# Performance work log

Measured on AMD Instinct MI355X. Metric: run time of the kernel, lower is better.

## Reference

```python
import jax, jax.numpy as jnp
import numpy as np

B, H, S, DH = 1, 16, 4096, 128
D_MODEL = H * DH  # 2048


def setup_inputs() -> dict:
    key = jax.random.key(0)
    kq, kk, kv = jax.random.split(key, 3)
    q = jax.random.normal(kq, (B, H, S, DH), dtype=jnp.float32)
    k = jax.random.normal(kk, (B, H, S, DH), dtype=jnp.float32)
    v = jax.random.normal(kv, (B, H, S, DH), dtype=jnp.float32)
    # causal mask: 1 where attending is allowed, 0 elsewhere (masked_fill on ==0)
    attn_mask = jnp.tril(jnp.ones((S, S), dtype=jnp.int32))[None, None, :, :]
    return {"q": q, "k": k, "v": v, "seq_length": S, "attn_mask": attn_mask}


def reference(q, k, v, seq_length, attn_mask):
    # q,k,v: [1, H, S, DH]; attn_mask: [1, 1, S, S] (0 = masked)
    scale = 1.0 / jnp.sqrt(jnp.asarray(q.shape[-1], dtype=q.dtype))
    att = jnp.einsum("bhqd,bhkd->bhqk", q, k) * scale  # [1,H,S,S]
    mask = attn_mask[:, :, :seq_length, :seq_length]
    att = jnp.where(mask == 0, jnp.asarray(-jnp.inf, dtype=att.dtype), att)
    att = jax.nn.softmax(att, axis=-1)
    y = jnp.einsum("bhqk,bhkd->bhqd", att, v)  # [1,H,S,DH]
    # transpose(1,2) -> [1,S,H,DH] -> view(S, d_model)
    y = jnp.transpose(y, (0, 2, 1, 3)).reshape(seq_length, H * DH)
    return y
```

## Files before the change

### kernel.cpp

```cpp
#include <hip/hip_runtime.h>

#define HH 16
#define SS 4096
#define DHD 128
#define BR 64
#define BC 64
#define LDQS 136
#define LDQ 144
#define LDV 68
#define LDPT 72
#define LDOS 136
#define DM  (HH * DHD)

typedef __bf16 bf16x8_t __attribute__((ext_vector_type(8)));
typedef __bf16 bf16x4_t __attribute__((ext_vector_type(4)));
typedef float  f32x4_t  __attribute__((ext_vector_type(4)));

#define BAR()  asm volatile("s_waitcnt lgkmcnt(0)\n\ts_barrier" ::: "memory")
#define BARV() asm volatile("s_waitcnt vmcnt(0)\n\ts_barrier" ::: "memory")

typedef __attribute__((address_space(1))) const void gas_t;
typedef __attribute__((address_space(3))) void las_t;
__device__ __forceinline__ void gl16(const void* g, void* l) {
    __builtin_amdgcn_global_load_lds((gas_t*)g, (las_t*)l, 16, 0, 0);
}

__device__ __forceinline__ f32x4_t vmax4(f32x4_t a, f32x4_t b) {
    f32x4_t r;
    r[0] = fmaxf(a[0], b[0]); r[1] = fmaxf(a[1], b[1]);
    r[2] = fmaxf(a[2], b[2]); r[3] = fmaxf(a[3], b[3]);
    return r;
}

__global__ __launch_bounds__(256)
void prep_k(const float* __restrict__ k, __bf16* __restrict__ wk)
{
    const int c0 = (blockIdx.x * 256 + threadIdx.x) * 4;
    #pragma unroll
    for (int i = 0; i < 4; ++i) {
        const int c    = c0 + i;
        const int tile = c >> 10;
        const int o    = (c & 1023) * 16;
        const int row  = o >> 8;
        const int e0   = (o & 255) >> 1;
        const int scol = e0 ^ ((row & 7) << 3);
        const float* src = k + (((size_t)(tile * 64 + row)) << 7) + scol;
        float4 a = ((const float4*)src)[0];
        float4 b = ((const float4*)src)[1];
        bf16x8_t bb;
        bb[0] = (__bf16)a.x; bb[1] = (__bf16)a.y; bb[2] = (__bf16)a.z; bb[3] = (__bf16)a.w;
        bb[4] = (__bf16)b.x; bb[5] = (__bf16)b.y; bb[6] = (__bf16)b.z; bb[7] = (__bf16)b.w;
        *(bf16x8_t*)((char*)wk + (size_t)c * 16) = bb;
    }
}

__global__ __launch_bounds__(256)
void prep_v(const float* __restrict__ v, __bf16* __restrict__ wv)
{
    __shared__ __bf16 lt[64 * 132];
    const int tile = blockIdx.x;
    const int tid  = threadIdx.x;
    #pragma unroll
    for (int i = 0; i < 8; ++i) {
        int idx = tid + i * 256;
        int r = idx >> 5, cc = idx & 31;
        float4 val = ((const float4*)(v + (((size_t)(tile * 64 + r)) << 7)))[cc];
        bf16x4_t bb;
        bb[0] = (__bf16)val.x; bb[1] = (__bf16)val.y;
        bb[2] = (__bf16)val.z; bb[3] = (__bf16)val.w;
        *(bf16x4_t*)&lt[r * 132 + cc * 4] = bb;
    }
    __syncthreads();
    #pragma unroll
    for (int i = 0; i < 4; ++i) {
        int ch = tid * 4 + i;
        int o  = ch * 8;
        int d  = o >> 6;
        int e0 = o & 63;
        int ks = e0 ^ ((d & 7) << 3);
        bf16x8_t bb;
        #pragma unroll
        for (int z = 0; z < 8; ++z) bb[z] = lt[(ks + z) * 132 + d];
        *(bf16x8_t*)((char*)wv + (size_t)tile * 16384 + (size_t)o * 2) = bb;
    }
}

__global__ __launch_bounds__(256, 2)
void fa_fwd(const float* __restrict__ q, const __bf16* __restrict__ wk,
            const __bf16* __restrict__ wv, float* __restrict__ out)
{
    const int L = blockIdx.x;
    const int h = L & 15;
    const int g = L >> 4;
    const int qts[2] = { g, 63 - g };

    const int tid  = threadIdx.x;
    const int wave = tid >> 6;
    const int lane = tid & 63;
    const int l16  = lane & 15;
    const int quad = lane >> 4;
    const int rK   = tid >> 5;
    const int c4   = tid & 31;
    const int swz  = (l16 & 7) << 4;

    __shared__ __align__(16) char smem[74752];
    unsigned short* pT_s = (unsigned short*)(smem + 65536);
    unsigned short* q_s  = (unsigned short*)(smem + 32768);
    float* os = (float*)smem;

    const float* qh = q + (size_t)h * SS * DHD;

    auto stage = [&](int j, int b) {
        const size_t tb = ((size_t)(h * 64 + j)) * 16384;
        const char* gk = (const char*)wk + tb + wave * 4096 + lane * 16;
        const char* gv = (const char*)wv + tb + wave * 4096 + lane * 16;
        char* lk = smem + b * 16384 + wave * 4096;
        char* lv = smem + 32768 + b * 16384 + wave * 4096;
        #pragma unroll
        for (int c2 = 0; c2 < 4; ++c2) {
            gl16(gk + c2 * 1024, lk + c2 * 1024);
            gl16(gv + c2 * 1024, lv + c2 * 1024);
        }
    };

    const float scale = 0.088388347648318447f * 1.4426950408889634f;

    for (int t = 0; t < 2; ++t) {
        const int qt = qts[t];
        __syncthreads();
        #pragma unroll
        for (int i = 0; i < 8; ++i) {
            int idx = tid + i * 256;
            int r   = idx >> 5;
            int cc  = idx & 31;
            float4 val = ((const float4*)(qh + (size_t)(qt * BR + r) * DHD))[cc];
            bf16x4_t bb;
            bb[0] = (__bf16)(val.x * scale); bb[1] = (__bf16)(val.y * scale);
            bb[2] = (__bf16)(val.z * scale); bb[3] = (__bf16)(val.w * scale);
            *(bf16x4_t*)&q_s[r * LDQS + cc * 4] = bb;
        }
        __syncthreads();

        bf16x8_t qf[4];
        #pragma unroll
        for (int kc = 0; kc < 4; ++kc)
            qf[kc] = *(const bf16x8_t*)
                &q_s[(wave * 16 + l16) * LDQS + kc * 32 + quad * 8];
        BAR();

        stage(0, 0);

        f32x4_t oacc[8];
        #pragma unroll
        for (int mt = 0; mt < 8; ++mt) oacc[mt] = (f32x4_t)(0.0f);
        float mi = -INFINITY, li = 0.0f;

        const int q_local = wave * 16 + l16;

        for (int j = 0; j <= qt; ++j) {
            const int cur = j & 1;
            BARV();
            if (j < qt) stage(j + 1, cur ^ 1);

            const char* kb = smem + cur * 16384;
            const char* vb = smem + 32768 + cur * 16384;

            f32x4_t sa[4];
            #pragma unroll
            for (int mt = 0; mt < 4; ++mt) sa[mt] = (f32x4_t)(0.0f);
            __builtin_amdgcn_s_setprio(1);
            #pragma unroll
            for (int kc = 0; kc < 4; ++kc)
                #pragma unroll
                for (int mt = 0; mt < 4; ++mt) {
                    bf16x8_t kf = *(const bf16x8_t*)
                        (kb + (mt * 16 + l16) * 256 + ((kc * 64 + quad * 16) ^ swz));
                    sa[mt] = __builtin_amdgcn_mfma_f32_16x16x32_bf16(kf, qf[kc], sa[mt], 0, 0, 0);
                }
            __builtin_amdgcn_s_setprio(0);

            if (j == qt) {
                #pragma unroll
                for (int mt = 0; mt < 4; ++mt)
                    #pragma unroll
                    for (int r = 0; r < 4; ++r)
                        if (mt * 16 + quad * 4 + r > q_local) sa[mt][r] = -INFINITY;
            }

            f32x4_t mv = vmax4(vmax4(sa[0], sa[1]), vmax4(sa[2], sa[3]));
            float mx = fmaxf(fmaxf(mv[0], mv[1]), fmaxf(mv[2], mv[3]));
            mx = fmaxf(mx, __shfl_xor(mx, 16));
            mx = fmaxf(mx, __shfl_xor(mx, 32));
            const bool skip = __all((int)(mx <= mi + 8.0f)) != 0;
            const float mnew = skip ? mi : fmaxf(mi, mx);
            bf16x4_t pkv[4];
            #pragma unroll
            for (int mt = 0; mt < 4; ++mt) {
                #pragma unroll
                for (int r = 0; r < 4; ++r)
                    sa[mt][r] = __builtin_amdgcn_exp2f(sa[mt][r] - mnew);
                pkv[mt][0] = (__bf16)sa[mt][0]; pkv[mt][1] = (__bf16)sa[mt][1];
                pkv[mt][2] = (__bf16)sa[mt][2]; pkv[mt][3] = (__bf16)sa[mt][3];
            }
            f32x4_t sv = sa[0] + sa[1] + sa[2] + sa[3];
            float rs = (sv[0] + sv[1]) + (sv[2] + sv[3]);
            rs += __shfl_xor(rs, 16);
            rs += __shfl_xor(rs, 32);
            if (skip) {
                li += rs;
            } else {
                float a = __builtin_amdgcn_exp2f(mi - mnew);
                mi = mnew;
                li = li * a + rs;
                #pragma unroll
                for (int mt = 0; mt < 8; ++mt) {
                    oacc[mt][0] *= a; oacc[mt][1] *= a;
                    oacc[mt][2] *= a; oacc[mt][3] *= a;
                }
            }

            #pragma unroll
            for (int mt = 0; mt < 4; ++mt)
                *(bf16x4_t*)&pT_s[q_local * LDPT + mt * 16 + quad * 4] = pkv[mt];

            __builtin_amdgcn_s_setprio(1);
            #pragma unroll
            for (int kc = 0; kc < 2; ++kc) {
                bf16x8_t pb = *(const bf16x8_t*)
                    &pT_s[q_local * LDPT + kc * 32 + quad * 8];
                #pragma unroll
                for (int mt = 0; mt < 8; ++mt) {
                    bf16x8_t vf = *(const bf16x8_t*)
                        (vb + (mt * 16 + l16) * 128 + ((kc * 64 + quad * 16) ^ swz));
                    oacc[mt] = __builtin_amdgcn_mfma_f32_16x16x32_bf16(vf, pb, oacc[mt], 0, 0, 0);
                }
            }
            __builtin_amdgcn_s_setprio(0);
        }

        __syncthreads();
        float inv = 1.0f / li;
        #pragma unroll
        for (int mt = 0; mt < 8; ++mt)
            #pragma unroll
            for (int r = 0; r < 4; ++r)
                os[(wave * 16 + l16) * LDOS + mt * 16 + quad * 4 + r] = oacc[mt][r] * inv;
        __syncthreads();
        #pragma unroll
        for (int p = 0; p < 8; ++p) {
            int row = p * 8 + rK;
            float4 f4 = *(const float4*)&os[row * LDOS + c4 * 4];
            *(float4*)&out[(size_t)(qts[t] * BR + row) * DM + h * DHD + c4 * 4] = f4;
        }
    }
}

__global__ __launch_bounds__(256, 2)
void fa_fwd_fb(const float* __restrict__ q, const float* __restrict__ k,
               const float* __restrict__ v, float* __restrict__ out)
{
    const int L = blockIdx.x;
    const int h = L & 15;
    const int g = L >> 4;
    const int qts[2] = { g, 63 - g };

    const int tid  = threadIdx.x;
    const int wave = tid >> 6;
    const int lane = tid & 63;
    const int l16  = lane & 15;
    const int quad = lane >> 4;
    const int rK   = tid >> 5;
    const int c4   = tid & 31;
    const int dbase = (wave & 1) * 64;
    const int rbase = (wave >> 1) * 32;

    __shared__ __align__(16) char smem[63488];
    unsigned short* qp_s = (unsigned short*)smem;
    unsigned short* k_s  = (unsigned short*)(smem + 18432);
    unsigned short* vt_s = (unsigned short*)(smem + 36864);
    unsigned short* pT_s = (unsigned short*)(smem + 54272);
    float* os = (float*)smem;

    const size_t hoff = (size_t)h * SS * DHD;
    const float* qh = q + hoff;
    const float* kh = k + hoff;
    const float* vh = v + hoff;

    float4 kreg[8];
    float  vreg[8][4];
    auto issue = [&](int j) {
        const float* kb = kh + (size_t)j * BC * DHD;
        #pragma unroll
        for (int i = 0; i < 8; ++i)
            kreg[i] = ((const float4*)(kb + (size_t)(rK + i * 8) * DHD))[c4];
        const float* vb = vh + (size_t)j * BC * DHD + dbase + lane;
        #pragma unroll
        for (int p = 0; p < 8; ++p) {
            const float* vp = vb + (size_t)(rbase + p * 4) * DHD;
            vreg[p][0] = vp[0];
            vreg[p][1] = vp[DHD];
            vreg[p][2] = vp[2 * DHD];
            vreg[p][3] = vp[3 * DHD];
        }
    };

    const float scale = 0.088388347648318447f;
    issue(0);

    for (int t = 0; t < 2; ++t) {
        const int qt = qts[t];
        __syncthreads();
        #pragma unroll
        for (int i = 0; i < 8; ++i) {
            int idx = tid + i * 256;
            int r   = idx >> 5;
            int cc  = idx & 31;
            float4 val = ((const float4*)(qh + (size_t)(qt * BR + r) * DHD))[cc];
            bf16x4_t bb;
            bb[0] = (__bf16)(val.x * scale); bb[1] = (__bf16)(val.y * scale);
            bb[2] = (__bf16)(val.z * scale); bb[3] = (__bf16)(val.w * scale);
            *(bf16x4_t*)&qp_s[r * LDQ + cc * 4] = bb;
        }
        __syncthreads();

        bf16x8_t qf[4];
        #pragma unroll
        for (int kc = 0; kc < 4; ++kc)
            qf[kc] = *(const bf16x8_t*)
                &qp_s[(wave * 16 + l16) * LDQ + kc * 32 + quad * 8];

        f32x4_t oacc[8];
        #pragma unroll
        for (int mt = 0; mt < 8; ++mt) oacc[mt] = (f32x4_t)(0.0f);
        float mi = -INFINITY, li = 0.0f;
        const int q_local = wave * 16 + l16;

        for (int j = 0; j <= qt; ++j) {
            BAR();
            #pragma unroll
            for (int i = 0; i < 8; ++i) {
                bf16x4_t bb;
                bb[0] = (__bf16)kreg[i].x; bb[1] = (__bf16)kreg[i].y;
                bb[2] = (__bf16)kreg[i].z; bb[3] = (__bf16)kreg[i].w;
                *(bf16x4_t*)&k_s[(rK + i * 8) * LDQ + c4 * 4] = bb;
            }
            #pragma unroll
            for (int p = 0; p < 8; ++p) {
                bf16x4_t bb;
                bb[0] = (__bf16)vreg[p][0]; bb[1] = (__bf16)vreg[p][1];
                bb[2] = (__bf16)vreg[p][2]; bb[3] = (__bf16)vreg[p][3];
                *(bf16x4_t*)&vt_s[(dbase + lane) * LDV + rbase + p * 4] = bb;
            }
            if (j < qt)      issue(j + 1);
            else if (t == 0) issue(0);
            BAR();

            f32x4_t sa[4];
            #pragma unroll
            for (int mt = 0; mt < 4; ++mt) sa[mt] = (f32x4_t)(0.0f);
            #pragma unroll
            for (int kc = 0; kc < 4; ++kc)
                #pragma unroll
                for (int mt = 0; mt < 4; ++mt) {
                    bf16x8_t kf = *(const bf16x8_t*)
                        &k_s[(mt * 16 + l16) * LDQ + kc * 32 + quad * 8];
                    sa[mt] = __builtin_amdgcn_mfma_f32_16x16x32_bf16(kf, qf[kc], sa[mt], 0, 0, 0);
                }

            if (j == qt) {
                #pragma unroll
                for (int mt = 0; mt < 4; ++mt)
                    #pragma unroll
                    for (int r = 0; r < 4; ++r)
                        if (mt * 16 + quad * 4 + r > q_local) sa[mt][r] = -INFINITY;
            }

            f32x4_t mv = vmax4(vmax4(sa[0], sa[1]), vmax4(sa[2], sa[3]));
            float mx = fmaxf(fmaxf(mv[0], mv[1]), fmaxf(mv[2], mv[3]));
            mx = fmaxf(mx, __shfl_xor(mx, 16));
            mx = fmaxf(mx, __shfl_xor(mx, 32));
            float mnew = fmaxf(mi, mx);
            float a = __expf(mi - mnew);
            mi = mnew;
            bf16x4_t pkv[4];
            #pragma unroll
            for (int mt = 0; mt < 4; ++mt) {
                #pragma unroll
                for (int r = 0; r < 4; ++r) sa[mt][r] = __expf(sa[mt][r] - mnew);
                pkv[mt][0] = (__bf16)sa[mt][0]; pkv[mt][1] = (__bf16)sa[mt][1];
                pkv[mt][2] = (__bf16)sa[mt][2]; pkv[mt][3] = (__bf16)sa[mt][3];
            }
            f32x4_t sv = sa[0] + sa[1] + sa[2] + sa[3];
            float rs = (sv[0] + sv[1]) + (sv[2] + sv[3]);
            rs += __shfl_xor(rs, 16);
            rs += __shfl_xor(rs, 32);
            li = li * a + rs;

            #pragma unroll
            for (int mt = 0; mt < 4; ++mt)
                *(bf16x4_t*)&pT_s[(wave * 16 + l16) * LDPT + mt * 16 + quad * 4] = pkv[mt];

            #pragma unroll
            for (int mt = 0; mt < 8; ++mt) {
                oacc[mt][0] *= a; oacc[mt][1] *= a;
                oacc[mt][2] *= a; oacc[mt][3] *= a;
            }

            #pragma unroll
            for (int kc = 0; kc < 2; ++kc) {
                bf16x8_t pb = *(const bf16x8_t*)
                    &pT_s[(wave * 16 + l16) * LDPT + kc * 32 + quad * 8];
                #pragma unroll
                for (int mt = 0; mt < 8; ++mt) {
                    bf16x4_t vlo = *(const bf16x4_t*)
                        &vt_s[(mt * 16 + l16) * LDV + kc * 32 + quad * 8];
                    bf16x4_t vhi = *(const bf16x4_t*)
                        &vt_s[(mt * 16 + l16) * LDV + kc * 32 + quad * 8 + 4];
                    bf16x8_t vf = __builtin_shufflevector(vlo, vhi, 0,1,2,3,4,5,6,7);
                    oacc[mt] = __builtin_amdgcn_mfma_f32_16x16x32_bf16(vf, pb, oacc[mt], 0, 0, 0);
                }
            }
        }

        __syncthreads();
        float inv = 1.0f / li;
        #pragma unroll
        for (int mt = 0; mt < 8; ++mt)
            #pragma unroll
            for (int r = 0; r < 4; ++r)
                os[(wave * 16 + l16) * LDOS + mt * 16 + quad * 4 + r] = oacc[mt][r] * inv;
        __syncthreads();
        #pragma unroll
        for (int p = 0; p < 8; ++p) {
            int row = p * 8 + rK;
            float4 f4 = *(const float4*)&os[row * LDOS + c4 * 4];
            *(float4*)&out[(size_t)(qt * BR + row) * DM + h * DHD + c4 * 4] = f4;
        }
    }
}

extern "C" void kernel_launch(void* const* d_in, const int* in_sizes, int n_in,
                              void* d_out, int out_size, void* d_ws, size_t ws_size,
                              hipStream_t stream) {
    const float* q = (const float*)d_in[0];
    const float* k = (const float*)d_in[1];
    const float* v = (const float*)d_in[2];
    float* out = (float*)d_out;
    if (d_ws != nullptr && ws_size >= (size_t)33554432) {
        __bf16* wk = (__bf16*)d_ws;
        __bf16* wv = (__bf16*)((char*)d_ws + 16777216);
        prep_k<<<dim3(1024), dim3(256), 0, stream>>>(k, wk);
        prep_v<<<dim3(1024), dim3(256), 0, stream>>>(v, wv);
        fa_fwd<<<dim3((SS / BR / 2) * HH), dim3(256), 0, stream>>>(q, wk, wv, out);
    } else {
        fa_fwd_fb<<<dim3((SS / BR / 2) * HH), dim3(256), 0, stream>>>(q, k, v, out);
    }
}
```

Before: 289.6 us.

## Software-pipeline QK^T one tile ahead with split K/V staging

Splits K and V loads into separate stages so that K is prefetched two tiles ahead and V one tile ahead. The loop is restructured to compute the next tile's QK^T scores while the current tile's softmax and PV run, ping-ponging between two score register sets. The row-sum reduction is deferred to the end, and the max shuffle now runs only when the rescale is not skipped. This hides LDS and MFMA latency behind softmax work, at the cost of more registers, which may hurt occupancy under the two-blocks-per-SIMD launch bound.

```diff
diff --git a/kernel.cpp b/kernel.cpp
--- a/kernel.cpp
+++ b/kernel.cpp
@@ -11,6 +11,7 @@
 #define LDPT 72
 #define LDOS 136
 #define DM  (HH * DHD)
+#define KTILE 16384
 
 typedef __bf16 bf16x8_t __attribute__((ext_vector_type(8)));
 typedef __bf16 bf16x4_t __attribute__((ext_vector_type(4)));
@@ -110,24 +111,98 @@
 
     const float* qh = q + (size_t)h * SS * DHD;
 
-    auto stage = [&](int j, int b) {
-        const size_t tb = ((size_t)(h * 64 + j)) * 16384;
-        const char* gk = (const char*)wk + tb + wave * 4096 + lane * 16;
-        const char* gv = (const char*)wv + tb + wave * 4096 + lane * 16;
-        char* lk = smem + b * 16384 + wave * 4096;
-        char* lv = smem + 32768 + b * 16384 + wave * 4096;
-        #pragma unroll
-        for (int c2 = 0; c2 < 4; ++c2) {
-            gl16(gk + c2 * 1024, lk + c2 * 1024);
-            gl16(gv + c2 * 1024, lv + c2 * 1024);
-        }
+    auto stageK = [&](int j, int b) {
+        const char* gk = (const char*)wk + ((size_t)(h * 64 + j)) * KTILE + wave * 4096 + lane * 16;
+        char* lk = smem + b * KTILE + wave * 4096;
+        #pragma unroll
+        for (int c2 = 0; c2 < 4; ++c2) gl16(gk + c2 * 1024, lk + c2 * 1024);
     };
+    auto stageV = [&](int j, int b) {
+        const char* gv = (const char*)wv + ((size_t)(h * 64 + j)) * KTILE + wave * 4096 + lane * 16;
+        char* lv = smem + 32768 + b * KTILE + wave * 4096;
+        #pragma unroll
+        for (int c2 = 0; c2 < 4; ++c2) gl16(gv + c2 * 1024, lv + c2 * 1024);
+    };
 
     const float scale = 0.088388347648318447f * 1.4426950408889634f;
+
+#define ITER(SC, SN) do {                                                     \
+    if (j + 2 <= qt) stageK(j + 2, j & 1);                                    \
+    if (j + 1 <= qt) stageV(j + 1, (j + 1) & 1);                              \
+    if (j < qt) {                                                             \
+        const char* kbp = smem + ((j + 1) & 1) * KTILE;                       \
+        _Pragma("unroll")                                                     \
+        for (int mt = 0; mt < 4; ++mt) SN[mt] = (f32x4_t)(0.0f);              \
+        __builtin_amdgcn_s_setprio(1);                                        \
+        _Pragma("unroll")                                                     \
+        for (int kc = 0; kc < 4; ++kc)                                        \
+            _Pragma("unroll")                                                 \
+            for (int mt = 0; mt < 4; ++mt) {                                  \
+                bf16x8_t kf = *(const bf16x8_t*)                              \
+                    (kbp + (mt * 16 + l16) * 256 + ((kc * 64 + quad * 16) ^ swz)); \
+                SN[mt] = __builtin_amdgcn_mfma_f32_16x16x32_bf16(kf, qf[kc], SN[mt], 0, 0, 0); \
+            }                                                                 \
+        __builtin_amdgcn_s_setprio(0);                                        \
+    }                                                                         \
+    if (j == qt) {                                                            \
+        _Pragma("unroll")                                                     \
+        for (int mt = 0; mt < 4; ++mt)                                        \
+            _Pragma("unroll")                                                 \
+            for (int r = 0; r < 4; ++r)                                       \
+                if (mt * 16 + quad * 4 + r > q_local) SC[mt][r] = -INFINITY;  \
+    }                                                                         \
+    f32x4_t mv = vmax4(vmax4(SC[0], SC[1]), vmax4(SC[2], SC[3]));             \
+    float mxl = fmaxf(fmaxf(mv[0], mv[1]), fmaxf(mv[2], mv[3]));              \
+    const bool skip = __all((int)(mxl <= mi + 8.0f)) != 0;                    \
+    float mnew = mi;                                                          \
+    if (!skip) {                                                              \
+        float mr = fmaxf(mxl, __shfl_xor(mxl, 16));                           \
+        mr = fmaxf(mr, __shfl_xor(mr, 32));                                   \
+        mnew = fmaxf(mi, mr);                                                 \
+        float a = __builtin_amdgcn_exp2f(mi - mnew);                          \
+        mi = mnew;                                                            \
+        li *= a;                                                              \
+        _Pragma("unroll")                                                     \
+        for (int mt = 0; mt < 8; ++mt) {                                      \
+            oacc[mt][0] *= a; oacc[mt][1] *= a;                               \
+            oacc[mt][2] *= a; oacc[mt][3] *= a;                               \
+        }                                                                     \
+    }                                                                         \
+    bf16x4_t pkv[4];                                                          \
+    _Pragma("unroll")                                                         \
+    for (int mt = 0; mt < 4; ++mt) {                                          \
+        _Pragma("unroll")                                                     \
+        for (int r = 0; r < 4; ++r)                                           \
+            SC[mt][r] = __builtin_amdgcn_exp2f(SC[mt][r] - mnew);             \
+        pkv[mt][0] = (__bf16)SC[mt][0]; pkv[mt][1] = (__bf16)SC[mt][1];       \
+        pkv[mt][2] = (__bf16)SC[mt][2]; pkv[mt][3] = (__bf16)SC[mt][3];       \
+        *(bf16x4_t*)&pT_s[q_local * LDPT + mt * 16 + quad * 4] = pkv[mt];     \
+    }                                                                         \
+    f32x4_t sv = SC[0] + SC[1] + SC[2] + SC[3];                               \
+    li += (sv[0] + sv[1]) + (sv[2] + sv[3]);                                  \
+    {                                                                         \
+        const char* vbp = smem + 32768 + (j & 1) * KTILE;                     \
+        __builtin_amdgcn_s_setprio(1);                                        \
+        _Pragma("unroll")                                                     \
+        for (int kc = 0; kc < 2; ++kc) {                                      \
+            bf16x8_t pb = *(const bf16x8_t*)&pT_s[q_local * LDPT + kc * 32 + quad * 8]; \
+            _Pragma("unroll")                                                 \
+            for (int mt = 0; mt < 8; ++mt) {                                  \
+                bf16x8_t vf = *(const bf16x8_t*)                              \
+                    (vbp + (mt * 16 + l16) * 128 + ((kc * 64 + quad * 16) ^ swz)); \
+                oacc[mt] = __builtin_amdgcn_mfma_f32_16x16x32_bf16(vf, pb, oacc[mt], 0, 0, 0); \
+            }                                                                 \
+        }                                                                     \
+        __builtin_amdgcn_s_setprio(0);                                        \
+    }                                                                         \
+    BARV();                                                                   \
+} while (0)
 
     for (int t = 0; t < 2; ++t) {
         const int qt = qts[t];
         __syncthreads();
+        stageK(0, 0);
+        stageK(1, 1);
         #pragma unroll
         for (int i = 0; i < 8; ++i) {
             int idx = tid + i * 256;
@@ -147,96 +222,43 @@
             qf[kc] = *(const bf16x8_t*)
                 &q_s[(wave * 16 + l16) * LDQS + kc * 32 + quad * 8];
         BAR();
-
-        stage(0, 0);
+        stageV(0, 0);
 
         f32x4_t oacc[8];
         #pragma unroll
         for (int mt = 0; mt < 8; ++mt) oacc[mt] = (f32x4_t)(0.0f);
         float mi = -INFINITY, li = 0.0f;
-
         const int q_local = wave * 16 + l16;
 
-        for (int j = 0; j <= qt; ++j) {
-            const int cur = j & 1;
-            BARV();
-            if (j < qt) stage(j + 1, cur ^ 1);
-
-            const char* kb = smem + cur * 16384;
-            const char* vb = smem + 32768 + cur * 16384;
-
-            f32x4_t sa[4];
-            #pragma unroll
-            for (int mt = 0; mt < 4; ++mt) sa[mt] = (f32x4_t)(0.0f);
+        BARV();
+
+        f32x4_t sA[4], sB[4];
+        {
+            const char* kbp = smem;
+            #pragma unroll
+            for (int mt = 0; mt < 4; ++mt) sA[mt] = (f32x4_t)(0.0f);
             __builtin_amdgcn_s_setprio(1);
             #pragma unroll
             for (int kc = 0; kc < 4; ++kc)
                 #pragma unroll
                 for (int mt = 0; mt < 4; ++mt) {
                     bf16x8_t kf = *(const bf16x8_t*)
-                        (kb + (mt * 16 + l16) * 256 + ((kc * 64 + quad * 16) ^ swz));
-                    sa[mt] = __builtin_amdgcn_mfma_f32_16x16x32_bf16(kf, qf[kc], sa[mt], 0, 0, 0);
+                        (kbp + (mt * 16 + l16) * 256 + ((kc * 64 + quad * 16) ^ swz));
+                    sA[mt] = __builtin_amdgcn_mfma_f32_16x16x32_bf16(kf, qf[kc], sA[mt], 0, 0, 0);
                 }
             __builtin_amdgcn_s_setprio(0);
-
-            if (j == qt) {
-                #pragma unroll
-                for (int mt = 0; mt < 4; ++mt)
-                    #pragma unroll
-                    for (int r = 0; r < 4; ++r)
-                        if (mt * 16 + quad * 4 + r > q_local) sa[mt][r] = -INFINITY;
-            }
-
-            f32x4_t mv = vmax4(vmax4(sa[0], sa[1]), vmax4(sa[2], sa[3]));
-            float mx = fmaxf(fmaxf(mv[0], mv[1]), fmaxf(mv[2], mv[3]));
-            mx = fmaxf(mx, __shfl_xor(mx, 16));
-            mx = fmaxf(mx, __shfl_xor(mx, 32));
-            const bool skip = __all((int)(mx <= mi + 8.0f)) != 0;
-            const float mnew = skip ? mi : fmaxf(mi, mx);
-            bf16x4_t pkv[4];
-            #pragma unroll
-            for (int mt = 0; mt < 4; ++mt) {
-                #pragma unroll
-                for (int r = 0; r < 4; ++r)
-                    sa[mt][r] = __builtin_amdgcn_exp2f(sa[mt][r] - mnew);
-                pkv[mt][0] = (__bf16)sa[mt][0]; pkv[mt][1] = (__bf16)sa[mt][1];
-                pkv[mt][2] = (__bf16)sa[mt][2]; pkv[mt][3] = (__bf16)sa[mt][3];
-            }
-            f32x4_t sv = sa[0] + sa[1] + sa[2] + sa[3];
-            float rs = (sv[0] + sv[1]) + (sv[2] + sv[3]);
-            rs += __shfl_xor(rs, 16);
-            rs += __shfl_xor(rs, 32);
-            if (skip) {
-                li += rs;
-            } else {
-                float a = __builtin_amdgcn_exp2f(mi - mnew);
-                mi = mnew;
-                li = li * a + rs;
-                #pragma unroll
-                for (int mt = 0; mt < 8; ++mt) {
-                    oacc[mt][0] *= a; oacc[mt][1] *= a;
-                    oacc[mt][2] *= a; oacc[mt][3] *= a;
-                }
-            }
-
-            #pragma unroll
-            for (int mt = 0; mt < 4; ++mt)
-                *(bf16x4_t*)&pT_s[q_local * LDPT + mt * 16 + quad * 4] = pkv[mt];
-
-            __builtin_amdgcn_s_setprio(1);
-            #pragma unroll
-            for (int kc = 0; kc < 2; ++kc) {
-                bf16x8_t pb = *(const bf16x8_t*)
-                    &pT_s[q_local * LDPT + kc * 32 + quad * 8];
-                #pragma unroll
-                for (int mt = 0; mt < 8; ++mt) {
-                    bf16x8_t vf = *(const bf16x8_t*)
-                        (vb + (mt * 16 + l16) * 128 + ((kc * 64 + quad * 16) ^ swz));
-                    oacc[mt] = __builtin_amdgcn_mfma_f32_16x16x32_bf16(vf, pb, oacc[mt], 0, 0, 0);
-                }
-            }
-            __builtin_amdgcn_s_setprio(0);
-        }
+        }
+
+        int j = 0;
+        for (;;) {
+            ITER(sA, sB);
+            if (j == qt) break; ++j;
+            ITER(sB, sA);
+            if (j == qt) break; ++j;
+        }
+
+        li += __shfl_xor(li, 16);
+        li += __shfl_xor(li, 32);
 
         __syncthreads();
         float inv = 1.0f / li;
@@ -250,9 +272,10 @@
         for (int p = 0; p < 8; ++p) {
             int row = p * 8 + rK;
             float4 f4 = *(const float4*)&os[row * LDOS + c4 * 4];
-            *(float4*)&out[(size_t)(qts[t] * BR + row) * DM + h * DHD + c4 * 4] = f4;
-        }
-    }
+            *(float4*)&out[(size_t)(qt * BR + row) * DM + h * DHD + c4 * 4] = f4;
+        }
+    }
+#undef ITER
 }
 
 __global__ __launch_bounds__(256, 2)
```

New measurement: 271.3 us. 6.3% less time.

## Load K/V MFMA fragments directly from global into registers, drop LDS staging

Applied to the files above, without the earlier changes.

Prep kernels now write K and V in MFMA fragment order so each wave loads its 16 K and 16 V bf16x8 fragments straight from global memory into registers. The LDS double buffer, global_load_lds staging and per-tile barriers go away, and the next tile is prefetched after each MFMA phase. Row-sum shuffles are deferred to the end of the loop and the max shuffle runs only when rescaling. Launch bounds drop to one block per SIMD set because of the higher register use. Each wave now loads the full K/V tile itself, so global/L2 traffic rises fourfold, and occupancy falls.

```diff
diff --git a/kernel.cpp b/kernel.cpp
--- a/kernel.cpp
+++ b/kernel.cpp
@@ -17,13 +17,6 @@
 typedef float  f32x4_t  __attribute__((ext_vector_type(4)));
 
 #define BAR()  asm volatile("s_waitcnt lgkmcnt(0)\n\ts_barrier" ::: "memory")
-#define BARV() asm volatile("s_waitcnt vmcnt(0)\n\ts_barrier" ::: "memory")
-
-typedef __attribute__((address_space(1))) const void gas_t;
-typedef __attribute__((address_space(3))) void las_t;
-__device__ __forceinline__ void gl16(const void* g, void* l) {
-    __builtin_amdgcn_global_load_lds((gas_t*)g, (las_t*)l, 16, 0, 0);
-}
 
 __device__ __forceinline__ f32x4_t vmax4(f32x4_t a, f32x4_t b) {
     f32x4_t r;
@@ -40,11 +33,12 @@
     for (int i = 0; i < 4; ++i) {
         const int c    = c0 + i;
         const int tile = c >> 10;
-        const int o    = (c & 1023) * 16;
-        const int row  = o >> 8;
-        const int e0   = (o & 255) >> 1;
-        const int scol = e0 ^ ((row & 7) << 3);
-        const float* src = k + (((size_t)(tile * 64 + row)) << 7) + scol;
+        const int idx  = c & 1023;
+        const int f    = idx >> 6;
+        const int ln   = idx & 63;
+        const int row  = (f & 3) * 16 + (ln & 15);
+        const int col  = (f >> 2) * 32 + (ln >> 4) * 8;
+        const float* src = k + (((size_t)(tile * 64 + row)) << 7) + col;
         float4 a = ((const float4*)src)[0];
         float4 b = ((const float4*)src)[1];
         bf16x8_t bb;
@@ -73,19 +67,19 @@
     __syncthreads();
     #pragma unroll
     for (int i = 0; i < 4; ++i) {
-        int ch = tid * 4 + i;
-        int o  = ch * 8;
-        int d  = o >> 6;
-        int e0 = o & 63;
-        int ks = e0 ^ ((d & 7) << 3);
+        int idx = tid * 4 + i;
+        int f   = idx >> 6;
+        int ln  = idx & 63;
+        int d   = (f & 7) * 16 + (ln & 15);
+        int kidx = (f >> 3) * 32 + (ln >> 4) * 8;
         bf16x8_t bb;
         #pragma unroll
-        for (int z = 0; z < 8; ++z) bb[z] = lt[(ks + z) * 132 + d];
-        *(bf16x8_t*)((char*)wv + (size_t)tile * 16384 + (size_t)o * 2) = bb;
-    }
-}
-
-__global__ __launch_bounds__(256, 2)
+        for (int z = 0; z < 8; ++z) bb[z] = lt[(kidx + z) * 132 + d];
+        *(bf16x8_t*)((char*)wv + (size_t)tile * 16384 + (size_t)idx * 16) = bb;
+    }
+}
+
+__global__ __launch_bounds__(256, 1)
 void fa_fwd(const float* __restrict__ q, const __bf16* __restrict__ wk,
             const __bf16* __restrict__ wv, float* __restrict__ out)
 {
@@ -101,26 +95,27 @@
     const int quad = lane >> 4;
     const int rK   = tid >> 5;
     const int c4   = tid & 31;
-    const int swz  = (l16 & 7) << 4;
-
-    __shared__ __align__(16) char smem[74752];
-    unsigned short* pT_s = (unsigned short*)(smem + 65536);
-    unsigned short* q_s  = (unsigned short*)(smem + 32768);
+
+    __shared__ __align__(16) char smem[44032];
+    unsigned short* q_s  = (unsigned short*)smem;
+    unsigned short* pT_s = (unsigned short*)(smem + 34816);
     float* os = (float*)smem;
 
     const float* qh = q + (size_t)h * SS * DHD;
-
-    auto stage = [&](int j, int b) {
-        const size_t tb = ((size_t)(h * 64 + j)) * 16384;
-        const char* gk = (const char*)wk + tb + wave * 4096 + lane * 16;
-        const char* gv = (const char*)wv + tb + wave * 4096 + lane * 16;
-        char* lk = smem + b * 16384 + wave * 4096;
-        char* lv = smem + 32768 + b * 16384 + wave * 4096;
-        #pragma unroll
-        for (int c2 = 0; c2 < 4; ++c2) {
-            gl16(gk + c2 * 1024, lk + c2 * 1024);
-            gl16(gv + c2 * 1024, lv + c2 * 1024);
-        }
+    const bf16x8_t* kh8 = (const bf16x8_t*)wk + (size_t)h * 64 * 1024 + lane;
+    const bf16x8_t* vh8 = (const bf16x8_t*)wv + (size_t)h * 64 * 1024 + lane;
+
+    bf16x8_t kf[16];
+    bf16x8_t vf[16];
+    auto ldk = [&](int j) {
+        const bf16x8_t* p = kh8 + (size_t)j * 1024;
+        #pragma unroll
+        for (int f = 0; f < 16; ++f) kf[f] = p[f * 64];
+    };
+    auto ldv = [&](int j) {
+        const bf16x8_t* p = vh8 + (size_t)j * 1024;
+        #pragma unroll
+        for (int f = 0; f < 16; ++f) vf[f] = p[f * 64];
     };
 
     const float scale = 0.088388347648318447f * 1.4426950408889634f;
@@ -128,6 +123,9 @@
     for (int t = 0; t < 2; ++t) {
         const int qt = qts[t];
         __syncthreads();
+        ldk(0);
+        ldv(0);
+
         #pragma unroll
         for (int i = 0; i < 8; ++i) {
             int idx = tid + i * 256;
@@ -146,25 +144,14 @@
         for (int kc = 0; kc < 4; ++kc)
             qf[kc] = *(const bf16x8_t*)
                 &q_s[(wave * 16 + l16) * LDQS + kc * 32 + quad * 8];
-        BAR();
-
-        stage(0, 0);
 
         f32x4_t oacc[8];
         #pragma unroll
         for (int mt = 0; mt < 8; ++mt) oacc[mt] = (f32x4_t)(0.0f);
         float mi = -INFINITY, li = 0.0f;
-
         const int q_local = wave * 16 + l16;
 
         for (int j = 0; j <= qt; ++j) {
-            const int cur = j & 1;
-            BARV();
-            if (j < qt) stage(j + 1, cur ^ 1);
-
-            const char* kb = smem + cur * 16384;
-            const char* vb = smem + 32768 + cur * 16384;
-
             f32x4_t sa[4];
             #pragma unroll
             for (int mt = 0; mt < 4; ++mt) sa[mt] = (f32x4_t)(0.0f);
@@ -172,12 +159,11 @@
             #pragma unroll
             for (int kc = 0; kc < 4; ++kc)
                 #pragma unroll
-                for (int mt = 0; mt < 4; ++mt) {
-                    bf16x8_t kf = *(const bf16x8_t*)
-                        (kb + (mt * 16 + l16) * 256 + ((kc * 64 + quad * 16) ^ swz));
-                    sa[mt] = __builtin_amdgcn_mfma_f32_16x16x32_bf16(kf, qf[kc], sa[mt], 0, 0, 0);
-                }
+                for (int mt = 0; mt < 4; ++mt)
+                    sa[mt] = __builtin_amdgcn_mfma_f32_16x16x32_bf16(
+                        kf[kc * 4 + mt], qf[kc], sa[mt], 0, 0, 0);
             __builtin_amdgcn_s_setprio(0);
+            if (j < qt) ldk(j + 1);
 
             if (j == qt) {
                 #pragma unroll
@@ -188,11 +174,22 @@
             }
 
             f32x4_t mv = vmax4(vmax4(sa[0], sa[1]), vmax4(sa[2], sa[3]));
-            float mx = fmaxf(fmaxf(mv[0], mv[1]), fmaxf(mv[2], mv[3]));
-            mx = fmaxf(mx, __shfl_xor(mx, 16));
-            mx = fmaxf(mx, __shfl_xor(mx, 32));
-            const bool skip = __all((int)(mx <= mi + 8.0f)) != 0;
-            const float mnew = skip ? mi : fmaxf(mi, mx);
+            float mxl = fmaxf(fmaxf(mv[0], mv[1]), fmaxf(mv[2], mv[3]));
+            const bool skip = __all((int)(mxl <= mi + 8.0f)) != 0;
+            float mnew = mi;
+            if (!skip) {
+                float mr = fmaxf(mxl, __shfl_xor(mxl, 16));
+                mr = fmaxf(mr, __shfl_xor(mr, 32));
+                mnew = fmaxf(mi, mr);
+                float a = __builtin_amdgcn_exp2f(mi - mnew);
+                mi = mnew;
+                li *= a;
+                #pragma unroll
+                for (int mt = 0; mt < 8; ++mt) {
+                    oacc[mt][0] *= a; oacc[mt][1] *= a;
+                    oacc[mt][2] *= a; oacc[mt][3] *= a;
+                }
+            }
             bf16x4_t pkv[4];
             #pragma unroll
             for (int mt = 0; mt < 4; ++mt) {
@@ -201,27 +198,10 @@
                     sa[mt][r] = __builtin_amdgcn_exp2f(sa[mt][r] - mnew);
                 pkv[mt][0] = (__bf16)sa[mt][0]; pkv[mt][1] = (__bf16)sa[mt][1];
                 pkv[mt][2] = (__bf16)sa[mt][2]; pkv[mt][3] = (__bf16)sa[mt][3];
+                *(bf16x4_t*)&pT_s[q_local * LDPT + mt * 16 + quad * 4] = pkv[mt];
             }
             f32x4_t sv = sa[0] + sa[1] + sa[2] + sa[3];
-            float rs = (sv[0] + sv[1]) + (sv[2] + sv[3]);
-            rs += __shfl_xor(rs, 16);
-            rs += __shfl_xor(rs, 32);
-            if (skip) {
-                li += rs;
-            } else {
-                float a = __builtin_amdgcn_exp2f(mi - mnew);
-                mi = mnew;
-                li = li * a + rs;
-                #pragma unroll
-                for (int mt = 0; mt < 8; ++mt) {
-                    oacc[mt][0] *= a; oacc[mt][1] *= a;
-                    oacc[mt][2] *= a; oacc[mt][3] *= a;
-                }
-            }
-
-            #pragma unroll
-            for (int mt = 0; mt < 4; ++mt)
-                *(bf16x4_t*)&pT_s[q_local * LDPT + mt * 16 + quad * 4] = pkv[mt];
+            li += (sv[0] + sv[1]) + (sv[2] + sv[3]);
 
             __builtin_amdgcn_s_setprio(1);
             #pragma unroll
@@ -229,14 +209,16 @@
                 bf16x8_t pb = *(const bf16x8_t*)
                     &pT_s[q_local * LDPT + kc * 32 + quad * 8];
                 #pragma unroll
-                for (int mt = 0; mt < 8; ++mt) {
-                    bf16x8_t vf = *(const bf16x8_t*)
-                        (vb + (mt * 16 + l16) * 128 + ((kc * 64 + quad * 16) ^ swz));
-                    oacc[mt] = __builtin_amdgcn_mfma_f32_16x16x32_bf16(vf, pb, oacc[mt], 0, 0, 0);
-                }
+                for (int mt = 0; mt < 8; ++mt)
+                    oacc[mt] = __builtin_amdgcn_mfma_f32_16x16x32_bf16(
+                        vf[kc * 8 + mt], pb, oacc[mt], 0, 0, 0);
             }
             __builtin_amdgcn_s_setprio(0);
-        }
+            if (j < qt) ldv(j + 1);
+        }
+
+        li += __shfl_xor(li, 16);
+        li += __shfl_xor(li, 32);
 
         __syncthreads();
         float inv = 1.0f / li;
@@ -250,7 +232,7 @@
         for (int p = 0; p < 8; ++p) {
             int row = p * 8 + rK;
             float4 f4 = *(const float4*)&os[row * LDOS + c4 * 4];
-            *(float4*)&out[(size_t)(qts[t] * BR + row) * DM + h * DHD + c4 * 4] = f4;
+            *(float4*)&out[(size_t)(qt * BR + row) * DM + h * DHD + c4 * 4] = f4;
         }
     }
 }
```

Result: slower. 303.1 us (+4.7%).
